# Kernel optimization log

Measured on AMD Instinct MI355X. Metric: run time of the kernel, lower is better.

## Reference

```python
import jax, jax.numpy as jnp
import numpy as np

N, D, V = 2048, 128, 131072
B, T = 8, 256
U_DECAY, X_DECAY, THR = 0.97, 0.97, 0.02


def _ln(z, eps=1e-6):
    # row-wise layernorm matching torch: std with ddof=1 (unbiased)
    m = z.mean(-1, keepdims=True)
    s = jnp.sqrt(((z - m) ** 2).sum(-1, keepdims=True) / (z.shape[-1] - 1))
    return (z - m) / (s + eps)


def setup_inputs() -> dict:
    key = jax.random.key(0)
    k = jax.random.split(key, 5)
    E = jax.random.normal(k[0], (D, N), dtype=jnp.float32) / N ** 0.5
    Dx = jax.random.normal(k[1], (N, D), dtype=jnp.float32) / D ** 0.5
    Dy = jax.random.normal(k[2], (N, D), dtype=jnp.float32) / D ** 0.5
    token_emb = jax.random.normal(k[3], (V, D), dtype=jnp.float32) / D ** 0.5
    tokens = jax.random.randint(k[4], (B, T), 0, V)
    return {"E": E, "Dx": Dx, "Dy": Dy, "token_emb": token_emb, "tokens": tokens}


def reference(E, Dx, Dy, token_emb, tokens):
    Bc, Tc = tokens.shape
    n, d = Dx.shape[0], Dx.shape[1]
    x0 = jnp.zeros((Bc, n), dtype=E.dtype)
    rho0 = jnp.zeros((Bc, d, n), dtype=E.dtype)

    def cell(carry, tok):
        x, rho = carry
        v_prev = token_emb[tok]                             # [B,d]
        xt = X_DECAY * x + v_prev @ Dx.T                    # [B,n]
        xt = xt / (jnp.abs(xt).sum(-1, keepdims=True) + 1e-6)
        thr = THR * xt.max(-1, keepdims=True)
        xt = jnp.where(xt > thr, xt, 0.0)                   # sparsifying threshold
        a_star = jnp.einsum('bdn,bn->bd', rho, xt)          # fast-weight read
        y_core = _ln(a_star) @ Dy.T                         # ln_before_Dy=True -> [B,n]
        yt = jnp.maximum(y_core, 0.0) * jnp.maximum(xt, 0.0)
        v_star = _ln(yt @ E.T)                              # [B,d]
        rho = U_DECAY * (rho + v_prev[:, :, None] * xt[:, None, :])  # rank-1 update + decay
        return (xt, rho), v_star

    (_, _), v_seq = jax.lax.scan(cell, (x0, rho0), tokens.T)  # v_seq: [T,B,d]
    return jnp.transpose(v_seq, (1, 0, 2))                    # [B,T,d]
```

## Files before the change

### kernel.cpp

```cpp
#include <hip/hip_runtime.h>

#define T_SEQ 256
#define N_DIM 2048
#define D_DIM 128
#define B_BATCH 8

__global__ __launch_bounds__(128) void k_gather(const float* __restrict__ emb,
                                                const int* __restrict__ toks,
                                                float* __restrict__ Vp) {
  int r = blockIdx.x;
  int d = threadIdx.x;
  int tok = toks[r];
  Vp[(long)r * D_DIM + d] = emb[(long)tok * D_DIM + d];
}

__global__ __launch_bounds__(256) void k_zero(float* __restrict__ p, long n4) {
  long i = (long)blockIdx.x * blockDim.x + threadIdx.x;
  if (i < n4) ((float4*)p)[i] = make_float4(0.f, 0.f, 0.f, 0.f);
}

template <int FUSE>
__global__ __launch_bounds__(256) void k_gemm_abT(
    const float* __restrict__ A, const float* __restrict__ Bm, float* __restrict__ C,
    int M, int N, int K, long sA, long sB, long sC, const float* __restrict__ Xr) {
  constexpr int BM = 64, BN = 64, BK = 16;
  A += (long)blockIdx.z * sA;
  Bm += (long)blockIdx.z * sB;
  C += (long)blockIdx.z * sC;
  const float* Xp = Xr ? Xr + (long)blockIdx.z * sC : nullptr;

  __shared__ float As[BK][BM + 4];
  __shared__ float Bs[BK][BN + 4];
  int tid = threadIdx.x;
  int tx = tid & 15, ty = tid >> 4;
  int row0 = blockIdx.y * BM, col0 = blockIdx.x * BN;
  float acc[4][4] = {};

  for (int k0 = 0; k0 < K; k0 += BK) {
#pragma unroll
    for (int i = 0; i < 4; i++) {
      int idx = tid + i * 256;
      int m = idx >> 4;
      int k = idx & 15;
      As[k][m] = A[(long)(row0 + m) * K + k0 + k];
      Bs[k][m] = Bm[(long)(col0 + m) * K + k0 + k];
    }
    __syncthreads();
#pragma unroll
    for (int k = 0; k < BK; k++) {
      float a[4], b[4];
#pragma unroll
      for (int i = 0; i < 4; i++) a[i] = As[k][ty * 4 + i];
#pragma unroll
      for (int j = 0; j < 4; j++) b[j] = Bs[k][tx * 4 + j];
#pragma unroll
      for (int i = 0; i < 4; i++)
#pragma unroll
        for (int j = 0; j < 4; j++) acc[i][j] += a[i] * b[j];
    }
    __syncthreads();
  }
#pragma unroll
  for (int i = 0; i < 4; i++) {
    long r = row0 + ty * 4 + i;
    long c = col0 + tx * 4;
    long off = r * (long)N + c;
    float4 v = make_float4(acc[i][0], acc[i][1], acc[i][2], acc[i][3]);
    if (FUSE) {
      float4 xv = *(const float4*)(Xp + off);
      v.x = fmaxf(v.x, 0.f) * fmaxf(xv.x, 0.f);
      v.y = fmaxf(v.y, 0.f) * fmaxf(xv.y, 0.f);
      v.z = fmaxf(v.z, 0.f) * fmaxf(xv.z, 0.f);
      v.w = fmaxf(v.w, 0.f) * fmaxf(xv.w, 0.f);
    }
    *(float4*)(C + off) = v;
  }
}

template <int TRI>
__global__ __launch_bounds__(256) void k_gemm_abT_splitk(
    const float* __restrict__ A, const float* __restrict__ Bm, float* __restrict__ C,
    int M, int N, int K, int KS, long sA, long sB, long sC) {
  constexpr int BM = 64, BN = 64, BK = 16;
  int bz = blockIdx.z;
  int batch = bz / KS, ks = bz - batch * KS;
  A += (long)batch * sA;
  Bm += (long)batch * sB;
  C += (long)batch * sC;
  int row0 = blockIdx.y * BM, col0 = blockIdx.x * BN;
  if (TRI && col0 > row0) return;
  int kLen = K / KS, k0beg = ks * kLen;

  __shared__ float As[BK][BM + 4];
  __shared__ float Bs[BK][BN + 4];
  int tid = threadIdx.x;
  int tx = tid & 15, ty = tid >> 4;
  float acc[4][4] = {};

  for (int k0 = k0beg; k0 < k0beg + kLen; k0 += BK) {
#pragma unroll
    for (int i = 0; i < 4; i++) {
      int idx = tid + i * 256;
      int m = idx >> 4;
      int k = idx & 15;
      As[k][m] = A[(long)(row0 + m) * K + k0 + k];
      Bs[k][m] = Bm[(long)(col0 + m) * K + k0 + k];
    }
    __syncthreads();
#pragma unroll
    for (int k = 0; k < BK; k++) {
      float a[4], b[4];
#pragma unroll
      for (int i = 0; i < 4; i++) a[i] = As[k][ty * 4 + i];
#pragma unroll
      for (int j = 0; j < 4; j++) b[j] = Bs[k][tx * 4 + j];
#pragma unroll
      for (int i = 0; i < 4; i++)
#pragma unroll
        for (int j = 0; j < 4; j++) acc[i][j] += a[i] * b[j];
    }
    __syncthreads();
  }
#pragma unroll
  for (int i = 0; i < 4; i++) {
    long r = row0 + ty * 4 + i;
    long c = col0 + tx * 4;
    float* cp = C + r * (long)N + c;
#pragma unroll
    for (int j = 0; j < 4; j++) unsafeAtomicAdd(cp + j, acc[i][j]);
  }
}

template <int CTRL>
__device__ __forceinline__ float dpp_mov(float v) {
  return __int_as_float(
      __builtin_amdgcn_update_dpp(0, __float_as_int(v), CTRL, 0xF, 0xF, true));
}

__device__ __forceinline__ void wave_reduce_sum_max63(float& s, float& m) {
  s += dpp_mov<0x111>(s);  m = fmaxf(m, dpp_mov<0x111>(m));
  s += dpp_mov<0x112>(s);  m = fmaxf(m, dpp_mov<0x112>(m));
  s += dpp_mov<0x114>(s);  m = fmaxf(m, dpp_mov<0x114>(m));
  s += dpp_mov<0x118>(s);  m = fmaxf(m, dpp_mov<0x118>(m));
  s += dpp_mov<0x142>(s);  m = fmaxf(m, dpp_mov<0x142>(m));
  s += dpp_mov<0x143>(s);  m = fmaxf(m, dpp_mov<0x143>(m));
}

__device__ __forceinline__ float wave_sum63(float s) {
  s += dpp_mov<0x111>(s);
  s += dpp_mov<0x112>(s);
  s += dpp_mov<0x114>(s);
  s += dpp_mov<0x118>(s);
  s += dpp_mov<0x142>(s);
  s += dpp_mov<0x143>(s);
  return s;
}

__global__ __launch_bounds__(256) void k_scan(const float* __restrict__ P,
                                              float* __restrict__ X) {
  int b = blockIdx.x;
  int tid = threadIdx.x;
  int wave = tid >> 6;
  int lane = tid & 63;
  __shared__ float red[2][4][2];

  const float4* Pv = (const float4*)(P + (long)b * T_SEQ * N_DIM);
  float4* Xv = (float4*)(X + (long)b * T_SEQ * N_DIM);
  const int ROWQ = N_DIM / 4;
  const long o0 = (long)tid * 2, o1 = o0 + 1;

  float x[8];
#pragma unroll
  for (int j = 0; j < 8; j++) x[j] = 0.f;

  auto rowOff = [&](int t) { return (long)(t < T_SEQ ? t : T_SEQ - 1) * ROWQ; };

  auto step = [&](const float4& v0, const float4& v1, int t) {
    float z[8];
    z[0] = 0.97f * x[0] + v0.x;
    z[1] = 0.97f * x[1] + v0.y;
    z[2] = 0.97f * x[2] + v0.z;
    z[3] = 0.97f * x[3] + v0.w;
    z[4] = 0.97f * x[4] + v1.x;
    z[5] = 0.97f * x[5] + v1.y;
    z[6] = 0.97f * x[6] + v1.z;
    z[7] = 0.97f * x[7] + v1.w;
    float s0 = fabsf(z[0]) + fabsf(z[4]);
    float s1 = fabsf(z[1]) + fabsf(z[5]);
    float s2 = fabsf(z[2]) + fabsf(z[6]);
    float s3 = fabsf(z[3]) + fabsf(z[7]);
    float m0 = fmaxf(z[0], z[4]);
    float m1 = fmaxf(z[1], z[5]);
    float m2 = fmaxf(z[2], z[6]);
    float m3 = fmaxf(z[3], z[7]);
    float s = (s0 + s1) + (s2 + s3);
    float m = fmaxf(fmaxf(m0, m1), fmaxf(m2, m3));
    wave_reduce_sum_max63(s, m);
    int par = t & 1;
    if (lane == 63) {
      red[par][wave][0] = s;
      red[par][wave][1] = m;
    }
    __syncthreads();
    float S = (red[par][0][0] + red[par][1][0]) + (red[par][2][0] + red[par][3][0]);
    float M = fmaxf(fmaxf(red[par][0][1], red[par][1][1]),
                    fmaxf(red[par][2][1], red[par][3][1]));
    float inv = 1.f / (S + 1e-6f);
    float thr = 0.02f * M;
#pragma unroll
    for (int j = 0; j < 8; j++) x[j] = (z[j] > thr) ? z[j] * inv : 0.f;
    long rb = (long)t * ROWQ;
    Xv[rb + o0] = make_float4(x[0], x[1], x[2], x[3]);
    Xv[rb + o1] = make_float4(x[4], x[5], x[6], x[7]);
  };

  float4 A0 = Pv[rowOff(0) + o0], A1 = Pv[rowOff(0) + o1];
  float4 B0 = Pv[rowOff(1) + o0], B1 = Pv[rowOff(1) + o1];
  float4 C0 = Pv[rowOff(2) + o0], C1 = Pv[rowOff(2) + o1];
  asm volatile("" ::: "memory");
  float4 D0, D1;

  for (int t = 0; t < T_SEQ; t += 4) {
    D0 = Pv[rowOff(t + 3) + o0];
    D1 = Pv[rowOff(t + 3) + o1];
    asm volatile("" ::: "memory");
    step(A0, A1, t);
    A0 = Pv[rowOff(t + 4) + o0];
    A1 = Pv[rowOff(t + 4) + o1];
    asm volatile("" ::: "memory");
    step(B0, B1, t + 1);
    B0 = Pv[rowOff(t + 5) + o0];
    B1 = Pv[rowOff(t + 5) + o1];
    asm volatile("" ::: "memory");
    step(C0, C1, t + 2);
    C0 = Pv[rowOff(t + 6) + o0];
    C1 = Pv[rowOff(t + 6) + o1];
    asm volatile("" ::: "memory");
    step(D0, D1, t + 3);
  }
}

__global__ __launch_bounds__(128) void k_astar_ln(const float* __restrict__ S,
                                                  const float* __restrict__ Vp,
                                                  float* __restrict__ LnA) {
  int bx = blockIdx.x;
  int b = bx >> 8, t = bx & 255;
  int d = threadIdx.x;
  int wave = d >> 6, lane = d & 63;
  __shared__ float redS[2], redV[2];
  const float* Sb = S + ((long)b * T_SEQ + t) * T_SEQ;
  const float* Vb = Vp + (long)b * T_SEQ * D_DIM;
  float acc = 0.f;
  float w = 1.f;
  for (int s = t - 1; s >= 0; s--) {
    w *= 0.97f;
    acc += w * Sb[s] * Vb[(long)s * D_DIM + d];
  }
  float s1 = wave_sum63(acc);
  if (lane == 63) redS[wave] = s1;
  __syncthreads();
  float mean = (redS[0] + redS[1]) * (1.f / 128.f);
  float dv = acc - mean;
  float v = wave_sum63(dv * dv);
  if (lane == 63) redV[wave] = v;
  __syncthreads();
  float sd = sqrtf((redV[0] + redV[1]) * (1.f / 127.f));
  LnA[((long)b * T_SEQ + t) * D_DIM + d] = dv / (sd + 1e-6f);
}

__global__ __launch_bounds__(64) void k_ln(const float* __restrict__ In,
                                           float* __restrict__ Out) {
  long base = (long)blockIdx.x * D_DIM;
  int lane = threadIdx.x;
  float a = In[base + lane];
  float b = In[base + lane + 64];
  float s = a + b;
#pragma unroll
  for (int off = 32; off >= 1; off >>= 1) s += __shfl_xor(s, off);
  float m = s * (1.f / 128.f);
  float da = a - m, db = b - m;
  float v = da * da + db * db;
#pragma unroll
  for (int off = 32; off >= 1; off >>= 1) v += __shfl_xor(v, off);
  float sd = sqrtf(v * (1.f / 127.f));
  float invs = 1.f / (sd + 1e-6f);
  Out[base + lane] = da * invs;
  Out[base + lane + 64] = db * invs;
}

extern "C" void kernel_launch(void* const* d_in, const int* in_sizes, int n_in,
                              void* d_out, int out_size, void* d_ws, size_t ws_size,
                              hipStream_t stream) {
  const float* E = (const float*)d_in[0];
  const float* Dx = (const float*)d_in[1];
  const float* Dy = (const float*)d_in[2];
  const float* emb = (const float*)d_in[3];
  const int* toks = (const int*)d_in[4];
  float* out = (float*)d_out;

  char* ws = (char*)d_ws;
  const size_t MB = 1u << 20;
  float* Vp = (float*)(ws + 0 * MB);
  float* P = (float*)(ws + 1 * MB);
  float* X = (float*)(ws + 17 * MB);
  float* S = (float*)(ws + 33 * MB);
  float* U = (float*)(ws + 35 * MB);
  float* LnA = (float*)(ws + 36 * MB);
  float* Yt = P;

  const int R = B_BATCH * T_SEQ;

  k_gather<<<R, D_DIM, 0, stream>>>(emb, toks, Vp);
  k_gemm_abT<0><<<dim3(N_DIM / 64, R / 64, 1), 256, 0, stream>>>(
      Vp, Dx, P, R, N_DIM, D_DIM, 0, 0, 0, nullptr);
  k_scan<<<B_BATCH, 256, 0, stream>>>(P, X);
  k_zero<<<768, 256, 0, stream>>>(S, 3L * MB / 16);
  k_gemm_abT_splitk<1><<<dim3(T_SEQ / 64, T_SEQ / 64, B_BATCH * 8), 256, 0, stream>>>(
      X, X, S, T_SEQ, T_SEQ, N_DIM, 8,
      (long)T_SEQ * N_DIM, (long)T_SEQ * N_DIM, (long)T_SEQ * T_SEQ);
  k_astar_ln<<<R, D_DIM, 0, stream>>>(S, Vp, LnA);
  k_gemm_abT<1><<<dim3(N_DIM / 64, R / 64, 1), 256, 0, stream>>>(
      LnA, Dy, Yt, R, N_DIM, D_DIM, 0, 0, 0, X);
  k_gemm_abT_splitk<0><<<dim3(D_DIM / 64, R / 64, 8), 256, 0, stream>>>(
      Yt, E, U, R, D_DIM, N_DIM, 8, 0, 0, 0);
  k_ln<<<R, 64, 0, stream>>>(U, out);
}
```

Before: 361.7 us.

## Switch three GEMMs to bf16 MFMA with bf16 intermediates

Three fp32 SIMT GEMMs are replaced by one templated kernel using bf16 16x16x32 MFMA and swizzled LDS tiles: the X·Xᵀ Gram product, the LnA·Dyᵀ product with its fused relu epilogue, and the Yt·Eᵀ product. X, LnA and Yt are now stored as bf16, and Dy and E are cast to bf16 on each call. This targets ALU-bound fp32 GEMM time and halves the intermediate memory traffic. The cost is two extra cast launches and the loss of precision from bf16 rounding.

```diff
diff --git a/kernel.cpp b/kernel.cpp
--- a/kernel.cpp
+++ b/kernel.cpp
@@ -1,9 +1,21 @@
 #include <hip/hip_runtime.h>
+
+typedef unsigned int u32;
+typedef unsigned short u16;
 
 #define T_SEQ 256
 #define N_DIM 2048
 #define D_DIM 128
 #define B_BATCH 8
+
+typedef __attribute__((ext_vector_type(8))) short bfrag;
+typedef __attribute__((ext_vector_type(4))) float f4acc;
+
+__device__ __forceinline__ u16 f2bf(float f) {
+  u32 u = __float_as_uint(f);
+  return (u16)((u + 0x7FFFu + ((u >> 16) & 1u)) >> 16);
+}
+__device__ __forceinline__ float bf2f(u16 h) { return __uint_as_float(((u32)h) << 16); }
 
 __global__ __launch_bounds__(128) void k_gather(const float* __restrict__ emb,
                                                 const int* __restrict__ toks,
@@ -14,21 +26,21 @@
   Vp[(long)r * D_DIM + d] = emb[(long)tok * D_DIM + d];
 }
 
+__global__ __launch_bounds__(256) void k_cast(const float* __restrict__ src,
+                                              u16* __restrict__ dst, int n) {
+  for (int i = blockIdx.x * 256 + threadIdx.x; i < n; i += gridDim.x * 256)
+    dst[i] = f2bf(src[i]);
+}
+
 __global__ __launch_bounds__(256) void k_zero(float* __restrict__ p, long n4) {
   long i = (long)blockIdx.x * blockDim.x + threadIdx.x;
   if (i < n4) ((float4*)p)[i] = make_float4(0.f, 0.f, 0.f, 0.f);
 }
 
-template <int FUSE>
 __global__ __launch_bounds__(256) void k_gemm_abT(
     const float* __restrict__ A, const float* __restrict__ Bm, float* __restrict__ C,
-    int M, int N, int K, long sA, long sB, long sC, const float* __restrict__ Xr) {
+    int M, int N, int K) {
   constexpr int BM = 64, BN = 64, BK = 16;
-  A += (long)blockIdx.z * sA;
-  Bm += (long)blockIdx.z * sB;
-  C += (long)blockIdx.z * sC;
-  const float* Xp = Xr ? Xr + (long)blockIdx.z * sC : nullptr;
-
   __shared__ float As[BK][BM + 4];
   __shared__ float Bs[BK][BN + 4];
   int tid = threadIdx.x;
@@ -62,73 +74,89 @@
   }
 #pragma unroll
   for (int i = 0; i < 4; i++) {
-    long r = row0 + ty * 4 + i;
-    long c = col0 + tx * 4;
-    long off = r * (long)N + c;
-    float4 v = make_float4(acc[i][0], acc[i][1], acc[i][2], acc[i][3]);
-    if (FUSE) {
-      float4 xv = *(const float4*)(Xp + off);
-      v.x = fmaxf(v.x, 0.f) * fmaxf(xv.x, 0.f);
-      v.y = fmaxf(v.y, 0.f) * fmaxf(xv.y, 0.f);
-      v.z = fmaxf(v.z, 0.f) * fmaxf(xv.z, 0.f);
-      v.w = fmaxf(v.w, 0.f) * fmaxf(xv.w, 0.f);
-    }
-    *(float4*)(C + off) = v;
-  }
-}
-
-template <int TRI>
-__global__ __launch_bounds__(256) void k_gemm_abT_splitk(
-    const float* __restrict__ A, const float* __restrict__ Bm, float* __restrict__ C,
-    int M, int N, int K, int KS, long sA, long sB, long sC) {
-  constexpr int BM = 64, BN = 64, BK = 16;
+    long off = (long)(row0 + ty * 4 + i) * N + col0 + tx * 4;
+    *(float4*)(C + off) = make_float4(acc[i][0], acc[i][1], acc[i][2], acc[i][3]);
+  }
+}
+
+template <int EPI, int TRI>
+__global__ __launch_bounds__(256) void k_mfma_abT(
+    const u16* __restrict__ A, const u16* __restrict__ Bm, void* __restrict__ Cv,
+    const u16* __restrict__ Xr, int M, int N, int K, int KS,
+    long sA, long sB, long sC) {
   int bz = blockIdx.z;
   int batch = bz / KS, ks = bz - batch * KS;
+  int row0 = blockIdx.y * 64, col0 = blockIdx.x * 64;
+  if (TRI && col0 > row0) return;
   A += (long)batch * sA;
   Bm += (long)batch * sB;
-  C += (long)batch * sC;
-  int row0 = blockIdx.y * BM, col0 = blockIdx.x * BN;
-  if (TRI && col0 > row0) return;
   int kLen = K / KS, k0beg = ks * kLen;
 
-  __shared__ float As[BK][BM + 4];
-  __shared__ float Bs[BK][BN + 4];
+  __shared__ __align__(16) u16 As[64 * 64];
+  __shared__ __align__(16) u16 Bs[64 * 64];
   int tid = threadIdx.x;
-  int tx = tid & 15, ty = tid >> 4;
-  float acc[4][4] = {};
-
-  for (int k0 = k0beg; k0 < k0beg + kLen; k0 += BK) {
-#pragma unroll
-    for (int i = 0; i < 4; i++) {
-      int idx = tid + i * 256;
-      int m = idx >> 4;
-      int k = idx & 15;
-      As[k][m] = A[(long)(row0 + m) * K + k0 + k];
-      Bs[k][m] = Bm[(long)(col0 + m) * K + k0 + k];
-    }
-    __syncthreads();
-#pragma unroll
-    for (int k = 0; k < BK; k++) {
-      float a[4], b[4];
-#pragma unroll
-      for (int i = 0; i < 4; i++) a[i] = As[k][ty * 4 + i];
-#pragma unroll
-      for (int j = 0; j < 4; j++) b[j] = Bs[k][tx * 4 + j];
-#pragma unroll
-      for (int i = 0; i < 4; i++)
-#pragma unroll
-        for (int j = 0; j < 4; j++) acc[i][j] += a[i] * b[j];
-    }
-    __syncthreads();
-  }
-#pragma unroll
-  for (int i = 0; i < 4; i++) {
-    long r = row0 + ty * 4 + i;
-    long c = col0 + tx * 4;
-    float* cp = C + r * (long)N + c;
-#pragma unroll
-    for (int j = 0; j < 4; j++) unsafeAtomicAdd(cp + j, acc[i][j]);
-  }
+  int w = tid >> 6, lane = tid & 63;
+  int qr = (w >> 1) * 32, qc = (w & 1) * 32;
+  int l15 = lane & 15, lhi = lane >> 4;
+
+  f4acc acc[2][2];
+#pragma unroll
+  for (int i = 0; i < 2; i++)
+#pragma unroll
+    for (int j = 0; j < 2; j++)
+#pragma unroll
+      for (int e = 0; e < 4; e++) acc[i][j][e] = 0.f;
+
+  for (int k0 = k0beg; k0 < k0beg + kLen; k0 += 64) {
+    __syncthreads();
+#pragma unroll
+    for (int p = 0; p < 2; p++) {
+      int idx = tid + p * 256;
+      int r = idx >> 3, c8 = (idx & 7) * 8;
+      uint4 av = *(const uint4*)(A + (long)(row0 + r) * K + k0 + c8);
+      uint4 bv = *(const uint4*)(Bm + (long)(col0 + r) * K + k0 + c8);
+      int sw = (c8 * 2) ^ ((r & 7) << 4);
+      *(uint4*)((char*)As + r * 128 + sw) = av;
+      *(uint4*)((char*)Bs + r * 128 + sw) = bv;
+    }
+    __syncthreads();
+#pragma unroll
+    for (int kk = 0; kk < 2; kk++) {
+      bfrag af[2], bf[2];
+      int cb = kk * 64 + lhi * 16;
+#pragma unroll
+      for (int f = 0; f < 2; f++) {
+        int ra = qr + f * 16 + l15;
+        af[f] = *(const bfrag*)((const char*)As + ra * 128 + (cb ^ ((ra & 7) << 4)));
+        int rb = qc + f * 16 + l15;
+        bf[f] = *(const bfrag*)((const char*)Bs + rb * 128 + (cb ^ ((rb & 7) << 4)));
+      }
+#pragma unroll
+      for (int i = 0; i < 2; i++)
+#pragma unroll
+        for (int j = 0; j < 2; j++)
+          acc[i][j] = __builtin_amdgcn_mfma_f32_16x16x32_bf16(af[i], bf[j], acc[i][j], 0, 0, 0);
+    }
+  }
+
+#pragma unroll
+  for (int i = 0; i < 2; i++)
+#pragma unroll
+    for (int j = 0; j < 2; j++) {
+      int rbase = row0 + qr + i * 16 + lhi * 4;
+      int c = col0 + qc + j * 16 + l15;
+#pragma unroll
+      for (int e = 0; e < 4; e++) {
+        long r = rbase + e;
+        float v = acc[i][j][e];
+        if (EPI == 0) {
+          unsafeAtomicAdd((float*)Cv + (long)batch * sC + r * N + c, v);
+        } else {
+          float xv = bf2f(Xr[r * (long)N + c]);
+          ((u16*)Cv)[r * (long)N + c] = f2bf(fmaxf(v, 0.f) * fmaxf(xv, 0.f));
+        }
+      }
+    }
 }
 
 template <int CTRL>
@@ -157,7 +185,7 @@
 }
 
 __global__ __launch_bounds__(256) void k_scan(const float* __restrict__ P,
-                                              float* __restrict__ X) {
+                                              u16* __restrict__ Xb) {
   int b = blockIdx.x;
   int tid = threadIdx.x;
   int wave = tid >> 6;
@@ -165,7 +193,7 @@
   __shared__ float red[2][4][2];
 
   const float4* Pv = (const float4*)(P + (long)b * T_SEQ * N_DIM);
-  float4* Xv = (float4*)(X + (long)b * T_SEQ * N_DIM);
+  u16* Xrow = Xb + (long)b * T_SEQ * N_DIM;
   const int ROWQ = N_DIM / 4;
   const long o0 = (long)tid * 2, o1 = o0 + 1;
 
@@ -209,40 +237,38 @@
     float thr = 0.02f * M;
 #pragma unroll
     for (int j = 0; j < 8; j++) x[j] = (z[j] > thr) ? z[j] * inv : 0.f;
-    long rb = (long)t * ROWQ;
-    Xv[rb + o0] = make_float4(x[0], x[1], x[2], x[3]);
-    Xv[rb + o1] = make_float4(x[4], x[5], x[6], x[7]);
+    uint4 pk;
+    pk.x = (u32)f2bf(x[0]) | ((u32)f2bf(x[1]) << 16);
+    pk.y = (u32)f2bf(x[2]) | ((u32)f2bf(x[3]) << 16);
+    pk.z = (u32)f2bf(x[4]) | ((u32)f2bf(x[5]) << 16);
+    pk.w = (u32)f2bf(x[6]) | ((u32)f2bf(x[7]) << 16);
+    *(uint4*)(Xrow + (long)t * N_DIM + tid * 8) = pk;
   };
 
   float4 A0 = Pv[rowOff(0) + o0], A1 = Pv[rowOff(0) + o1];
   float4 B0 = Pv[rowOff(1) + o0], B1 = Pv[rowOff(1) + o1];
   float4 C0 = Pv[rowOff(2) + o0], C1 = Pv[rowOff(2) + o1];
-  asm volatile("" ::: "memory");
   float4 D0, D1;
 
   for (int t = 0; t < T_SEQ; t += 4) {
     D0 = Pv[rowOff(t + 3) + o0];
     D1 = Pv[rowOff(t + 3) + o1];
-    asm volatile("" ::: "memory");
     step(A0, A1, t);
     A0 = Pv[rowOff(t + 4) + o0];
     A1 = Pv[rowOff(t + 4) + o1];
-    asm volatile("" ::: "memory");
     step(B0, B1, t + 1);
     B0 = Pv[rowOff(t + 5) + o0];
     B1 = Pv[rowOff(t + 5) + o1];
-    asm volatile("" ::: "memory");
     step(C0, C1, t + 2);
     C0 = Pv[rowOff(t + 6) + o0];
     C1 = Pv[rowOff(t + 6) + o1];
-    asm volatile("" ::: "memory");
     step(D0, D1, t + 3);
   }
 }
 
 __global__ __launch_bounds__(128) void k_astar_ln(const float* __restrict__ S,
                                                   const float* __restrict__ Vp,
-                                                  float* __restrict__ LnA) {
+                                                  u16* __restrict__ LnAb) {
   int bx = blockIdx.x;
   int b = bx >> 8, t = bx & 255;
   int d = threadIdx.x;
@@ -265,7 +291,7 @@
   if (lane == 63) redV[wave] = v;
   __syncthreads();
   float sd = sqrtf((redV[0] + redV[1]) * (1.f / 127.f));
-  LnA[((long)b * T_SEQ + t) * D_DIM + d] = dv / (sd + 1e-6f);
+  LnAb[((long)b * T_SEQ + t) * D_DIM + d] = f2bf(dv / (sd + 1e-6f));
 }
 
 __global__ __launch_bounds__(64) void k_ln(const float* __restrict__ In,
@@ -302,26 +328,30 @@
   const size_t MB = 1u << 20;
   float* Vp = (float*)(ws + 0 * MB);
   float* P = (float*)(ws + 1 * MB);
-  float* X = (float*)(ws + 17 * MB);
-  float* S = (float*)(ws + 33 * MB);
-  float* U = (float*)(ws + 35 * MB);
-  float* LnA = (float*)(ws + 36 * MB);
-  float* Yt = P;
+  u16* Ytb = (u16*)(ws + 1 * MB);
+  u16* Xb = (u16*)(ws + 17 * MB);
+  float* S = (float*)(ws + 25 * MB);
+  float* U = (float*)(ws + 27 * MB);
+  u16* LnAb = (u16*)(ws + 28 * MB);
+  u16* Dyb = (u16*)(ws + 29 * MB);
+  u16* Eb = (u16*)(ws + 30 * MB);
 
   const int R = B_BATCH * T_SEQ;
 
   k_gather<<<R, D_DIM, 0, stream>>>(emb, toks, Vp);
-  k_gemm_abT<0><<<dim3(N_DIM / 64, R / 64, 1), 256, 0, stream>>>(
-      Vp, Dx, P, R, N_DIM, D_DIM, 0, 0, 0, nullptr);
-  k_scan<<<B_BATCH, 256, 0, stream>>>(P, X);
+  k_cast<<<256, 256, 0, stream>>>(Dy, Dyb, N_DIM * D_DIM);
+  k_cast<<<256, 256, 0, stream>>>(E, Eb, N_DIM * D_DIM);
+  k_gemm_abT<<<dim3(N_DIM / 64, R / 64, 1), 256, 0, stream>>>(
+      Vp, Dx, P, R, N_DIM, D_DIM);
+  k_scan<<<B_BATCH, 256, 0, stream>>>(P, Xb);
   k_zero<<<768, 256, 0, stream>>>(S, 3L * MB / 16);
-  k_gemm_abT_splitk<1><<<dim3(T_SEQ / 64, T_SEQ / 64, B_BATCH * 8), 256, 0, stream>>>(
-      X, X, S, T_SEQ, T_SEQ, N_DIM, 8,
+  k_mfma_abT<0, 1><<<dim3(4, 4, B_BATCH * 4), 256, 0, stream>>>(
+      Xb, Xb, S, nullptr, T_SEQ, T_SEQ, N_DIM, 4,
       (long)T_SEQ * N_DIM, (long)T_SEQ * N_DIM, (long)T_SEQ * T_SEQ);
-  k_astar_ln<<<R, D_DIM, 0, stream>>>(S, Vp, LnA);
-  k_gemm_abT<1><<<dim3(N_DIM / 64, R / 64, 1), 256, 0, stream>>>(
-      LnA, Dy, Yt, R, N_DIM, D_DIM, 0, 0, 0, X);
-  k_gemm_abT_splitk<0><<<dim3(D_DIM / 64, R / 64, 8), 256, 0, stream>>>(
-      Yt, E, U, R, D_DIM, N_DIM, 8, 0, 0, 0);
+  k_astar_ln<<<R, D_DIM, 0, stream>>>(S, Vp, LnAb);
+  k_mfma_abT<1, 0><<<dim3(N_DIM / 64, R / 64, 1), 256, 0, stream>>>(
+      LnAb, Dyb, Ytb, Xb, R, N_DIM, D_DIM, 1, 0, 0, 0);
+  k_mfma_abT<0, 0><<<dim3(D_DIM / 64, R / 64, 8), 256, 0, stream>>>(
+      Ytb, Eb, U, nullptr, R, D_DIM, N_DIM, 8, 0, 0, 0);
   k_ln<<<R, 64, 0, stream>>>(U, out);
 }
```

Result: faster. 297.9 us (-17.7%).
